# Kernel tuning notes

Measured on AMD Instinct MI355X. Metric: run time of the kernel, lower is better.

Reference implementation:

```python
import jax, jax.numpy as jnp
import numpy as np
from jax import lax

NUM_KERNELS = 256
B, C, L = 128, 10, 16384
EPS = 1e-10
NORMALIZE = True
KERNEL_LENGTHS = np.array([7, 9, 11])


def _make_kernel_meta():
    """Deterministic ROCKET-style ragged kernel metadata (static ints)."""
    rng = np.random.default_rng(0)
    lengths = rng.choice(KERNEL_LENGTHS, NUM_KERNELS).astype(np.int64)
    nci = rng.integers(1, C + 1, NUM_KERNELS).astype(np.int64)  # channels per kernel
    channel_indices = np.concatenate(
        [rng.choice(C, int(n), replace=False) for n in nci]).astype(np.int64)
    dilations = np.array(
        [int(2 ** rng.uniform(0.0, np.log2((L - 1) / (l - 1)))) for l in lengths],
        dtype=np.int64)
    paddings = np.array(
        [((l - 1) * d) // 2 if rng.integers(2) else 0 for l, d in zip(lengths, dilations)],
        dtype=np.int64)
    return lengths, nci, channel_indices, dilations, paddings


def setup_inputs() -> dict:
    lengths, nci, channel_indices, dilations, paddings = _make_kernel_meta()
    total_w = int(np.sum(lengths * nci))
    key = jax.random.key(0)
    kx, kw, kb = jax.random.split(key, 3)
    x = jax.random.normal(kx, (B, C, L), dtype=jnp.float32)
    weights = jax.random.normal(kw, (total_w,), dtype=jnp.float32)
    biases = jax.random.uniform(kb, (NUM_KERNELS,), minval=-1.0, maxval=1.0,
                                dtype=jnp.float32)
    return {
        'x': x,
        'weights': weights,
        'biases': biases,
        'lengths': jnp.asarray(lengths),
        'dilations': jnp.asarray(dilations),
        'paddings': jnp.asarray(paddings),
        'num_channel_indices': jnp.asarray(nci),
        'channel_indices': jnp.asarray(channel_indices),
    }


def reference(x, weights, biases, lengths, dilations, paddings,
              num_channel_indices, channel_indices):
    # Ragged metadata must be static (defines per-kernel shapes).
    lengths = np.asarray(lengths)
    dilations = np.asarray(dilations)
    paddings = np.asarray(paddings)
    nci = np.asarray(num_channel_indices)
    channel_indices = np.asarray(channel_indices)
    windices = np.concatenate([[0], np.cumsum(lengths * nci)])
    cindices = np.concatenate([[0], np.cumsum(nci)])

    if NORMALIZE:
        mean_ = jnp.mean(x, axis=-1, keepdims=True)
        std_ = jnp.std(x, axis=-1, keepdims=True, ddof=1)  # torch unbiased std
        x = (x - mean_) / (std_ + EPS)

    ppvs, mxs = [], []
    for k in range(NUM_KERNELS):
        w = weights[windices[k]:windices[k + 1]].reshape(int(nci[k]), int(lengths[k]))
        chans = channel_indices[cindices[k]:cindices[k + 1]]
        px = x[:, chans, :]                       # [B, c_k, L]
        d, p = int(dilations[k]), int(paddings[k])
        yy = lax.conv_general_dilated(
            px, w[None],                          # rhs: [1, c_k, len_k]
            window_strides=(1,), padding=[(p, p)], rhs_dilation=(d,),
            dimension_numbers=('NCH', 'OIH', 'NCH'))[:, 0, :] + biases[k]  # [B, Lout]
        ppvs.append(jnp.mean((yy > 0).astype(x.dtype), axis=-1))
        sm = jax.nn.softmax(yy * 1000.0, axis=-1)  # sharp softmax ~ smooth max
        mxs.append(jnp.sum(sm * yy, axis=-1))

    ppv = jnp.stack(ppvs, axis=1)                 # [B, K]
    mx = jnp.stack(mxs, axis=1)                   # [B, K]
    # interleave: y[:, 2k] = ppv_k, y[:, 2k+1] = mx_k
    return jnp.stack([ppv, mx], axis=2).reshape(x.shape[0], 2 * NUM_KERNELS)
```

## Files before the change

kernel.cpp:

```cpp
#include <hip/hip_runtime.h>

#define NK 256
#define BB 128
#define CC 10
#define LL 16384
#define EPSV 1e-10f
#define GS2 15
#define XW 1792
#define WROW 12

__device__ __forceinline__ void block_finish(int cnt, float mx,
                                             float* rm, int* rc,
                                             int Lout, float* out, int b, int k) {
    int tid = threadIdx.x;
    for (int off = 32; off; off >>= 1) {
        mx = fmaxf(mx, __shfl_down(mx, off));
        cnt += __shfl_down(cnt, off);
    }
    int wv = tid >> 6, ln = tid & 63;
    if (ln == 0) { rm[wv] = mx; rc[wv] = cnt; }
    __syncthreads();
    if (tid == 0) {
#pragma unroll
        for (int i = 1; i < 4; ++i) { mx = fmaxf(mx, rm[i]); cnt += rc[i]; }
        size_t o = (size_t)b * (2 * NK) + 2 * k;
        out[o] = (float)cnt / (float)Lout;
        out[o + 1] = mx;
    }
}

__global__ __launch_bounds__(256) void stats_kernel(const float* __restrict__ x,
                                                    float* __restrict__ wsf) {
    int row = blockIdx.x;
    const float4* x4 = (const float4*)(x + (size_t)row * LL);
    int tid = threadIdx.x;
    float s = 0.f, s2 = 0.f;
    for (int i = tid; i < LL / 4; i += 256) {
        float4 v = x4[i];
        s += v.x + v.y + v.z + v.w;
        s2 += v.x * v.x + v.y * v.y + v.z * v.z + v.w * v.w;
    }
    for (int off = 32; off; off >>= 1) {
        s += __shfl_down(s, off);
        s2 += __shfl_down(s2, off);
    }
    __shared__ float as_[4], as2_[4];
    int wv = tid >> 6, ln = tid & 63;
    if (ln == 0) { as_[wv] = s; as2_[wv] = s2; }
    __syncthreads();
    if (tid == 0) {
        float S = as_[0] + as_[1] + as_[2] + as_[3];
        float S2 = as2_[0] + as2_[1] + as2_[2] + as2_[3];
        float mean = S / (float)LL;
        float var = (S2 - (float)LL * mean * mean) / (float)(LL - 1);
        var = fmaxf(var, 0.f);
        float inv = 1.f / (sqrtf(var) + EPSV);
        wsf[row] = inv;
        wsf[1280 + row] = -mean * inv;
    }
}

__global__ __launch_bounds__(256) void prefix_kernel(const int* __restrict__ lengths,
                                                     const int* __restrict__ ncis,
                                                     int* __restrict__ wbase,
                                                     int* __restrict__ cbase) {
    __shared__ int s1[NK], s2[NK];
    int k = threadIdx.x;
    int v1 = lengths[k] * ncis[k];
    int v2 = ncis[k];
    s1[k] = v1; s2[k] = v2;
    for (int off = 1; off < NK; off <<= 1) {
        __syncthreads();
        int a = (k >= off) ? s1[k - off] : 0;
        int b = (k >= off) ? s2[k - off] : 0;
        __syncthreads();
        s1[k] += a; s2[k] += b;
    }
    __syncthreads();
    wbase[k] = s1[k] - v1;
    cbase[k] = s2[k] - v2;
}

template <int LEN>
__device__ __forceinline__ void conv_S(
    const float* __restrict__ x, float* __restrict__ xw,
    const float* __restrict__ wsmR, const float* __restrict__ wsmS,
    const int* __restrict__ choff, const float* __restrict__ cinv,
    const float* __restrict__ csh,
    int d, int ms, int Lout, int nci, float biasE, float biasI,
    int wu, int lane, int& cnt, float& mx) {
    constexpr int W = GS2 + LEN - 1;
    const int qpt = 64 / d;
    const int MT = qpt * GS2;
    const int stot = d * (MT + LEN - 1);
    const int nit4 = (stot + 3 + 255) >> 8;
    const int nitS = (stot + 3 + 63) >> 6;
    const int Qmax = (Lout + d - 1) / d;
    const int nqt = (Qmax + MT - 1) / MT;
    int qi = lane / d, rho = lane - qi * d;
    bool act = qi < qpt;
    int a0 = act ? qi * GS2 * d + rho : 0;
    float rv[28];

    for (int j = wu; j < nqt; j += 4) {
        int qt = j * MT;
        int tb = (qt - ms) * d;
        int off = tb & 3, base = tb - off;
        bool interior = (base >= 0) && (base + (nit4 << 8) <= LL);
        float acc[GS2];
#pragma unroll
        for (int g = 0; g < GS2; ++g) acc[g] = 0.f;

        if (interior) {
            {
                const float* xp = x + choff[0] + base + 4 * lane;
#pragma unroll
                for (int it = 0; it < 7; ++it)
                    if (it < nit4) *(float4*)&rv[4 * it] = *(const float4*)(xp + (it << 8));
            }
            for (int ci = 0; ci < nci; ++ci) {
#pragma unroll
                for (int it = 0; it < 7; ++it)
                    if (it < nit4) *(float4*)&xw[4 * lane + (it << 8)] = *(const float4*)&rv[4 * it];
                if (ci + 1 < nci) {
                    const float* xp = x + choff[ci + 1] + base + 4 * lane;
#pragma unroll
                    for (int it = 0; it < 7; ++it)
                        if (it < nit4) *(float4*)&rv[4 * it] = *(const float4*)(xp + (it << 8));
                }
                float wreg[WROW];
                const float4* wv4 = (const float4*)&wsmS[ci * WROW];
#pragma unroll
                for (int u = 0; u < (LEN + 3) / 4; ++u) {
                    float4 w4 = wv4[u];
                    wreg[4 * u + 0] = w4.x; wreg[4 * u + 1] = w4.y;
                    wreg[4 * u + 2] = w4.z; wreg[4 * u + 3] = w4.w;
                }
                float win[W];
                int a = off + a0;
#pragma unroll
                for (int i = 0; i < W; ++i) { win[i] = xw[a]; a += d; }
#pragma unroll
                for (int jj = 0; jj < LEN; ++jj)
#pragma unroll
                    for (int g = 0; g < GS2; ++g)
                        acc[g] = fmaf(wreg[jj], win[g + jj], acc[g]);
            }
        } else {
            {
                const float* xc = x + choff[0];
#pragma unroll
                for (int it = 0; it < 26; ++it)
                    if (it < nitS) {
                        int t = base + (it << 6) + lane;
                        t = t < 0 ? 0 : (t > LL - 1 ? LL - 1 : t);
                        rv[it] = xc[t];
                    }
            }
            for (int ci = 0; ci < nci; ++ci) {
                float inv = cinv[ci], sh = csh[ci];
#pragma unroll
                for (int it = 0; it < 26; ++it)
                    if (it < nitS) {
                        int t = base + (it << 6) + lane;
                        float v = ((unsigned)t < (unsigned)LL) ? fmaf(rv[it], inv, sh) : 0.f;
                        xw[(it << 6) + lane] = v;
                    }
                if (ci + 1 < nci) {
                    const float* xc = x + choff[ci + 1];
#pragma unroll
                    for (int it = 0; it < 26; ++it)
                        if (it < nitS) {
                            int t = base + (it << 6) + lane;
                            t = t < 0 ? 0 : (t > LL - 1 ? LL - 1 : t);
                            rv[it] = xc[t];
                        }
                }
                float wreg[WROW];
                const float4* wv4 = (const float4*)&wsmR[ci * WROW];
#pragma unroll
                for (int u = 0; u < (LEN + 3) / 4; ++u) {
                    float4 w4 = wv4[u];
                    wreg[4 * u + 0] = w4.x; wreg[4 * u + 1] = w4.y;
                    wreg[4 * u + 2] = w4.z; wreg[4 * u + 3] = w4.w;
                }
                float win[W];
                int a = off + a0;
#pragma unroll
                for (int i = 0; i < W; ++i) { win[i] = xw[a]; a += d; }
#pragma unroll
                for (int jj = 0; jj < LEN; ++jj)
#pragma unroll
                    for (int g = 0; g < GS2; ++g)
                        acc[g] = fmaf(wreg[jj], win[g + jj], acc[g]);
            }
        }

        float bt = interior ? biasI : biasE;
        if (act) {
            int qb = qt + qi * GS2;
            if ((qb + GS2) * d <= Lout) {
                float am = acc[0];
#pragma unroll
                for (int g = 1; g < GS2; ++g) am = fmaxf(am, acc[g]);
                mx = fmaxf(mx, am + bt);
                float nb = -bt;
#pragma unroll
                for (int g = 0; g < GS2; ++g) cnt += (acc[g] > nb) ? 1 : 0;
            } else {
#pragma unroll
                for (int g = 0; g < GS2; ++g) {
                    int t = (qb + g) * d + rho;
                    if (t < Lout) {
                        float y = acc[g] + bt;
                        cnt += (y > 0.f) ? 1 : 0;
                        mx = fmaxf(mx, y);
                    }
                }
            }
        }
    }
}

template <int LEN, int GG>
__device__ __forceinline__ void conv_T(
    const float* __restrict__ x,
    const float* __restrict__ wsmR, const float* __restrict__ wsmS,
    const int* __restrict__ choff, const float* __restrict__ cinv,
    const float* __restrict__ csh,
    int d, int ms, int Lout, int nci, float biasE, float biasI,
    int wu, int lane, int& cnt, float& mx) {
    constexpr int M = GG + LEN - 1;
    const int Qmax = (Lout + d - 1) / d;
    const int nqt = (Qmax + GG - 1) / GG;
    const int nch = (d + 63) >> 6;
    const int T = nch * nqt;

    int qj = 0, c = wu;
    while (c >= nch) { c -= nch; ++qj; }

    for (int j = wu; j < T; j += 4) {
        int qb0 = qj * GG;
        int rho = (c << 6) + lane;
        bool actT = rho < d;
        int m0 = qb0 - ms;
        int tl = m0 * d + rho;
        int tminU = m0 * d + (c << 6);
        bool interior = (tminU >= 0) && (tminU + 63 + (M - 1) * d < LL);
        float acc[GG];
#pragma unroll
        for (int g = 0; g < GG; ++g) acc[g] = 0.f;

        float rA[M], rB[M];

        if (interior) {
            {
                const float* xc = x + choff[0];
                int t = tl;
#pragma unroll
                for (int m = 0; m < M; ++m) { rA[m] = xc[t]; t += d; }
            }
            int ci = 0;
            while (true) {
                if (ci + 1 < nci) {
                    const float* xc = x + choff[ci + 1];
                    int t = tl;
#pragma unroll
                    for (int m = 0; m < M; ++m) { rB[m] = xc[t]; t += d; }
                }
                {
                    float wreg[WROW];
                    const float4* wv4 = (const float4*)&wsmS[ci * WROW];
#pragma unroll
                    for (int u = 0; u < (LEN + 3) / 4; ++u) {
                        float4 w4 = wv4[u];
                        wreg[4 * u + 0] = w4.x; wreg[4 * u + 1] = w4.y;
                        wreg[4 * u + 2] = w4.z; wreg[4 * u + 3] = w4.w;
                    }
#pragma unroll
                    for (int jj = 0; jj < LEN; ++jj)
#pragma unroll
                        for (int g = 0; g < GG; ++g)
                            acc[g] = fmaf(wreg[jj], rA[g + jj], acc[g]);
                }
                ++ci; if (ci >= nci) break;
                if (ci + 1 < nci) {
                    const float* xc = x + choff[ci + 1];
                    int t = tl;
#pragma unroll
                    for (int m = 0; m < M; ++m) { rA[m] = xc[t]; t += d; }
                }
                {
                    float wreg[WROW];
                    const float4* wv4 = (const float4*)&wsmS[ci * WROW];
#pragma unroll
                    for (int u = 0; u < (LEN + 3) / 4; ++u) {
                        float4 w4 = wv4[u];
                        wreg[4 * u + 0] = w4.x; wreg[4 * u + 1] = w4.y;
                        wreg[4 * u + 2] = w4.z; wreg[4 * u + 3] = w4.w;
                    }
#pragma unroll
                    for (int jj = 0; jj < LEN; ++jj)
#pragma unroll
                        for (int g = 0; g < GG; ++g)
                            acc[g] = fmaf(wreg[jj], rB[g + jj], acc[g]);
                }
                ++ci; if (ci >= nci) break;
            }
        } else {
            {
                const float* xc = x + choff[0];
                int t = tl;
#pragma unroll
                for (int m = 0; m < M; ++m) {
                    int tc = t < 0 ? 0 : (t > LL - 1 ? LL - 1 : t);
                    rA[m] = xc[tc]; t += d;
                }
            }
            int ci = 0;
            while (true) {
                if (ci + 1 < nci) {
                    const float* xc = x + choff[ci + 1];
                    int t = tl;
#pragma unroll
                    for (int m = 0; m < M; ++m) {
                        int tc = t < 0 ? 0 : (t > LL - 1 ? LL - 1 : t);
                        rB[m] = xc[tc]; t += d;
                    }
                }
                {
                    float inv = cinv[ci], sh = csh[ci];
                    int t = tl;
#pragma unroll
                    for (int m = 0; m < M; ++m) {
                        rA[m] = ((unsigned)t < (unsigned)LL) ? fmaf(rA[m], inv, sh) : 0.f;
                        t += d;
                    }
                    float wreg[WROW];
                    const float4* wv4 = (const float4*)&wsmR[ci * WROW];
#pragma unroll
                    for (int u = 0; u < (LEN + 3) / 4; ++u) {
                        float4 w4 = wv4[u];
                        wreg[4 * u + 0] = w4.x; wreg[4 * u + 1] = w4.y;
                        wreg[4 * u + 2] = w4.z; wreg[4 * u + 3] = w4.w;
                    }
#pragma unroll
                    for (int jj = 0; jj < LEN; ++jj)
#pragma unroll
                        for (int g = 0; g < GG; ++g)
                            acc[g] = fmaf(wreg[jj], rA[g + jj], acc[g]);
                }
                ++ci; if (ci >= nci) break;
                if (ci + 1 < nci) {
                    const float* xc = x + choff[ci + 1];
                    int t = tl;
#pragma unroll
                    for (int m = 0; m < M; ++m) {
                        int tc = t < 0 ? 0 : (t > LL - 1 ? LL - 1 : t);
                        rA[m] = xc[tc]; t += d;
                    }
                }
                {
                    float inv = cinv[ci], sh = csh[ci];
                    int t = tl;
#pragma unroll
                    for (int m = 0; m < M; ++m) {
                        rB[m] = ((unsigned)t < (unsigned)LL) ? fmaf(rB[m], inv, sh) : 0.f;
                        t += d;
                    }
                    float wreg[WROW];
                    const float4* wv4 = (const float4*)&wsmR[ci * WROW];
#pragma unroll
                    for (int u = 0; u < (LEN + 3) / 4; ++u) {
                        float4 w4 = wv4[u];
                        wreg[4 * u + 0] = w4.x; wreg[4 * u + 1] = w4.y;
                        wreg[4 * u + 2] = w4.z; wreg[4 * u + 3] = w4.w;
                    }
#pragma unroll
                    for (int jj = 0; jj < LEN; ++jj)
#pragma unroll
                        for (int g = 0; g < GG; ++g)
                            acc[g] = fmaf(wreg[jj], rB[g + jj], acc[g]);
                }
                ++ci; if (ci >= nci) break;
            }
        }

        float bt = interior ? biasI : biasE;
        if (actT) {
            if ((qb0 + GG) * d <= Lout) {
                float am = acc[0];
#pragma unroll
                for (int g = 1; g < GG; ++g) am = fmaxf(am, acc[g]);
                mx = fmaxf(mx, am + bt);
                float nb = -bt;
#pragma unroll
                for (int g = 0; g < GG; ++g) cnt += (acc[g] > nb) ? 1 : 0;
            } else {
#pragma unroll
                for (int g = 0; g < GG; ++g) {
                    int t = (qb0 + g) * d + rho;
                    if (t < Lout) {
                        float y = acc[g] + bt;
                        cnt += (y > 0.f) ? 1 : 0;
                        mx = fmaxf(mx, y);
                    }
                }
            }
        }
        c += 4;
        while (c >= nch) { c -= nch; ++qj; }
    }
}

__global__ __launch_bounds__(256) void conv_kernel(
    const float* __restrict__ x, const float* __restrict__ weights,
    const float* __restrict__ biases,
    const int* __restrict__ lengths, const int* __restrict__ dil,
    const int* __restrict__ pad, const int* __restrict__ ncis,
    const int* __restrict__ chidx,
    const float* __restrict__ wsf, const int* __restrict__ wbase,
    const int* __restrict__ cbase, float* __restrict__ out) {
    int k = blockIdx.x, b = blockIdx.y;
    __shared__ __align__(16) float xl[4 * XW];
    __shared__ __align__(16) float wsmR[CC * WROW];
    __shared__ __align__(16) float wsmS[CC * WROW];
    __shared__ int choff[CC];
    __shared__ float cinv[CC], csh[CC];
    __shared__ float rm[4];
    __shared__ int rc[4];

    int tid = threadIdx.x;
    int len = lengths[k], d = dil[k], p = pad[k], nci = ncis[k];
    int wb = wbase[k], cb = cbase[k];

    if (tid < nci) {
        int ch = chidx[cb + tid];
        choff[tid] = (b * CC + ch) * LL;
        cinv[tid] = wsf[b * CC + ch];
        csh[tid] = wsf[1280 + b * CC + ch];
    }
    __syncthreads();
    for (int i = tid; i < nci * WROW; i += 256) {
        int ci = i / WROW, jj = i - ci * WROW;
        float wv = (jj < len) ? weights[wb + ci * len + jj] : 0.f;
        wsmR[i] = wv;
        wsmS[i] = wv * cinv[ci];
    }
    __syncthreads();

    float csum = 0.f;
    for (int ci = 0; ci < nci; ++ci) {
        float sw = 0.f;
        for (int jj = 0; jj < WROW; ++jj) sw += wsmR[ci * WROW + jj];
        csum += csh[ci] * sw;
    }

    int span = (len - 1) * d;
    int Lout = LL + 2 * p - span;
    int ms = p / d;
    float biasE = biases[k];
    float biasI = biasE + csum;
    int Qmax = (Lout + d - 1) / d;

    int wu = tid >> 6;
    int lane = tid & 63;
    float* xw = xl + wu * XW;
    int cnt = 0;
    float mx = -3.4e38f;

    if (d <= 64) {
        switch (len) {
            case 7:  conv_S<7>(x, xw, wsmR, wsmS, choff, cinv, csh, d, ms, Lout, nci, biasE, biasI, wu, lane, cnt, mx); break;
            case 9:  conv_S<9>(x, xw, wsmR, wsmS, choff, cinv, csh, d, ms, Lout, nci, biasE, biasI, wu, lane, cnt, mx); break;
            default: conv_S<11>(x, xw, wsmR, wsmS, choff, cinv, csh, d, ms, Lout, nci, biasE, biasI, wu, lane, cnt, mx); break;
        }
    } else if (Qmax > 12) {
        switch (len) {
            case 7:  conv_T<7, 16>(x, wsmR, wsmS, choff, cinv, csh, d, ms, Lout, nci, biasE, biasI, wu, lane, cnt, mx); break;
            case 9:  conv_T<9, 16>(x, wsmR, wsmS, choff, cinv, csh, d, ms, Lout, nci, biasE, biasI, wu, lane, cnt, mx); break;
            default: conv_T<11, 16>(x, wsmR, wsmS, choff, cinv, csh, d, ms, Lout, nci, biasE, biasI, wu, lane, cnt, mx); break;
        }
    } else {
        switch (len) {
            case 7:  conv_T<7, 4>(x, wsmR, wsmS, choff, cinv, csh, d, ms, Lout, nci, biasE, biasI, wu, lane, cnt, mx); break;
            case 9:  conv_T<9, 4>(x, wsmR, wsmS, choff, cinv, csh, d, ms, Lout, nci, biasE, biasI, wu, lane, cnt, mx); break;
            default: conv_T<11, 4>(x, wsmR, wsmS, choff, cinv, csh, d, ms, Lout, nci, biasE, biasI, wu, lane, cnt, mx); break;
        }
    }
    block_finish(cnt, mx, rm, rc, Lout, out, b, k);
}

extern "C" void kernel_launch(void* const* d_in, const int* in_sizes, int n_in,
                              void* d_out, int out_size, void* d_ws, size_t ws_size,
                              hipStream_t stream) {
    const float* x = (const float*)d_in[0];
    const float* weights = (const float*)d_in[1];
    const float* biases = (const float*)d_in[2];
    const int* lengths = (const int*)d_in[3];
    const int* dil = (const int*)d_in[4];
    const int* pad = (const int*)d_in[5];
    const int* ncis = (const int*)d_in[6];
    const int* chidx = (const int*)d_in[7];
    float* out = (float*)d_out;

    float* wsf = (float*)d_ws;
    int* wbase = (int*)((char*)d_ws + 2560 * sizeof(float));
    int* cbase = wbase + NK;

    stats_kernel<<<dim3(BB * CC), dim3(256), 0, stream>>>(x, wsf);
    prefix_kernel<<<dim3(1), dim3(256), 0, stream>>>(lengths, ncis, wbase, cbase);
    dim3 grid(NK, BB);
    conv_kernel<<<grid, dim3(256), 0, stream>>>(x, weights, biases, lengths, dil,
                                                pad, ncis, chidx, wsf, wbase,
                                                cbase, out);
}
```

Measured before the change: 2.348 ms.

## Flatten conv_T work mapping to dense lane indices and add setprio around FMA blocks

Replaces the per-wave (channel-chunk, q-tile) iteration in conv_T, which left lanes idle whenever the dilation was not a multiple of 64, with a flat index over d*nqt outputs. Each lane now gets a distinct (q, rho) pair. Interior detection becomes a per-lane check combined with a wave-wide __all vote. It also wraps the inner FMA loops in s_setprio(1)/s_setprio(0) to favour waves that are issuing math. The cost is an unsigned division per iteration, and with the new mapping lanes in one wave may access scattered positions, which can hurt coalescing.

```diff
diff --git a/kernel.cpp b/kernel.cpp
--- a/kernel.cpp
+++ b/kernel.cpp
@@ -140,11 +140,13 @@
                 int a = off + a0;
 #pragma unroll
                 for (int i = 0; i < W; ++i) { win[i] = xw[a]; a += d; }
+                __builtin_amdgcn_s_setprio(1);
 #pragma unroll
                 for (int jj = 0; jj < LEN; ++jj)
 #pragma unroll
                     for (int g = 0; g < GS2; ++g)
                         acc[g] = fmaf(wreg[jj], win[g + jj], acc[g]);
+                __builtin_amdgcn_s_setprio(0);
             }
         } else {
             {
@@ -188,11 +190,13 @@
                 int a = off + a0;
 #pragma unroll
                 for (int i = 0; i < W; ++i) { win[i] = xw[a]; a += d; }
+                __builtin_amdgcn_s_setprio(1);
 #pragma unroll
                 for (int jj = 0; jj < LEN; ++jj)
 #pragma unroll
                     for (int g = 0; g < GS2; ++g)
                         acc[g] = fmaf(wreg[jj], win[g + jj], acc[g]);
+                __builtin_amdgcn_s_setprio(0);
             }
         }
 
@@ -233,20 +237,18 @@
     constexpr int M = GG + LEN - 1;
     const int Qmax = (Lout + d - 1) / d;
     const int nqt = (Qmax + GG - 1) / GG;
-    const int nch = (d + 63) >> 6;
-    const int T = nch * nqt;
-
-    int qj = 0, c = wu;
-    while (c >= nch) { c -= nch; ++qj; }
-
-    for (int j = wu; j < T; j += 4) {
-        int qb0 = qj * GG;
-        int rho = (c << 6) + lane;
-        bool actT = rho < d;
-        int m0 = qb0 - ms;
-        int tl = m0 * d + rho;
-        int tminU = m0 * d + (c << 6);
-        bool interior = (tminU >= 0) && (tminU + 63 + (M - 1) * d < LL);
+    const int NT = d * nqt;
+
+    for (int f0 = wu * 64; f0 < NT; f0 += 256) {
+        int f = f0 + lane;
+        bool active = f < NT;
+        int fc = active ? f : NT - 1;
+        unsigned qi = (unsigned)fc / (unsigned)d;
+        int rho = fc - (int)qi * d;
+        int qb0 = (int)qi * GG;
+        int tl = (qb0 - ms) * d + rho;
+        bool laneInt = (tl >= 0) && (tl + (M - 1) * d < LL);
+        bool interior = __all(laneInt);
         float acc[GG];
 #pragma unroll
         for (int g = 0; g < GG; ++g) acc[g] = 0.f;
@@ -277,11 +279,13 @@
                         wreg[4 * u + 0] = w4.x; wreg[4 * u + 1] = w4.y;
                         wreg[4 * u + 2] = w4.z; wreg[4 * u + 3] = w4.w;
                     }
+                    __builtin_amdgcn_s_setprio(1);
 #pragma unroll
                     for (int jj = 0; jj < LEN; ++jj)
 #pragma unroll
                         for (int g = 0; g < GG; ++g)
                             acc[g] = fmaf(wreg[jj], rA[g + jj], acc[g]);
+                    __builtin_amdgcn_s_setprio(0);
                 }
                 ++ci; if (ci >= nci) break;
                 if (ci + 1 < nci) {
@@ -299,11 +303,13 @@
                         wreg[4 * u + 0] = w4.x; wreg[4 * u + 1] = w4.y;
                         wreg[4 * u + 2] = w4.z; wreg[4 * u + 3] = w4.w;
                     }
+                    __builtin_amdgcn_s_setprio(1);
 #pragma unroll
                     for (int jj = 0; jj < LEN; ++jj)
 #pragma unroll
                         for (int g = 0; g < GG; ++g)
                             acc[g] = fmaf(wreg[jj], rB[g + jj], acc[g]);
+                    __builtin_amdgcn_s_setprio(0);
                 }
                 ++ci; if (ci >= nci) break;
             }
@@ -344,11 +350,13 @@
                         wreg[4 * u + 0] = w4.x; wreg[4 * u + 1] = w4.y;
                         wreg[4 * u + 2] = w4.z; wreg[4 * u + 3] = w4.w;
                     }
+                    __builtin_amdgcn_s_setprio(1);
 #pragma unroll
                     for (int jj = 0; jj < LEN; ++jj)
 #pragma unroll
                         for (int g = 0; g < GG; ++g)
                             acc[g] = fmaf(wreg[jj], rA[g + jj], acc[g]);
+                    __builtin_amdgcn_s_setprio(0);
                 }
                 ++ci; if (ci >= nci) break;
                 if (ci + 1 < nci) {
@@ -376,18 +384,20 @@
                         wreg[4 * u + 0] = w4.x; wreg[4 * u + 1] = w4.y;
                         wreg[4 * u + 2] = w4.z; wreg[4 * u + 3] = w4.w;
                     }
+                    __builtin_amdgcn_s_setprio(1);
 #pragma unroll
                     for (int jj = 0; jj < LEN; ++jj)
 #pragma unroll
                         for (int g = 0; g < GG; ++g)
                             acc[g] = fmaf(wreg[jj], rB[g + jj], acc[g]);
+                    __builtin_amdgcn_s_setprio(0);
                 }
                 ++ci; if (ci >= nci) break;
             }
         }
 
         float bt = interior ? biasI : biasE;
-        if (actT) {
+        if (active) {
             if ((qb0 + GG) * d <= Lout) {
                 float am = acc[0];
 #pragma unroll
@@ -408,8 +418,6 @@
                 }
             }
         }
-        c += 4;
-        while (c >= nch) { c -= nch; ++qj; }
     }
 }
 
```

Result: no change. 2.322 ms (-1.1%).
